# Performance work log

Measured on AMD Instinct MI355X. Metric: run time of the kernel, lower is better.

Reference implementation:

```python
import jax, jax.numpy as jnp
import numpy as np

DECAY_INIT = 0.9
SPECTRAL_RADIUS = 0.5
EPS = 1e-8


def _spectral_normed(W, u, radius):
    # 3 power iterations (no-grad in torch); u, v treated as constants.
    for _ in range(3):
        v = W.T @ u
        v = v / (jnp.linalg.norm(v) + EPS)
        u = W @ v
        u = u / (jnp.linalg.norm(u) + EPS)
    u = jax.lax.stop_gradient(u)
    v = jax.lax.stop_gradient(v)
    sigma = jnp.abs(u @ W @ v)
    return W * (radius / (sigma + EPS))


def setup_inputs() -> dict:
    key = jax.random.key(0)
    ks = jax.random.split(key, 6)
    T, B, D, n = 2048, 8, 1024, 64
    xavier = float(np.sqrt(2.0 / (D + n)))
    x = jax.random.normal(ks[0], (T, B, D), dtype=jnp.float32)
    S0 = jnp.zeros((B, n, n), dtype=jnp.float32)
    W_k = jax.random.normal(ks[1], (n, D), dtype=jnp.float32) * xavier
    W_v = jax.random.normal(ks[2], (n, D), dtype=jnp.float32) * xavier
    W_q = jax.random.normal(ks[3], (n, D), dtype=jnp.float32) * xavier
    u_k = jax.random.normal(ks[4], (n,), dtype=jnp.float32)
    u_k = u_k / (jnp.linalg.norm(u_k) + EPS)
    u_v = jax.random.normal(ks[5], (n,), dtype=jnp.float32)
    u_v = u_v / (jnp.linalg.norm(u_v) + EPS)
    return {"x": x, "S0": S0, "W_k": W_k, "W_v": W_v, "W_q": W_q,
            "u_k": u_k, "u_v": u_v}


def reference(x, S0, W_k, W_v, W_q, u_k, u_v):
    # decay = clamp(0.9, 0, 0.999).item() -> detached constant
    decay = jnp.clip(jnp.float32(DECAY_INIT), 0.0, 0.999)
    Wk = _spectral_normed(W_k, u_k, SPECTRAL_RADIUS)
    Wv = _spectral_normed(W_v, u_v, SPECTRAL_RADIUS)

    # projections: [T, B, n]
    k_all = jnp.einsum('tbd,nd->tbn', x, Wk)
    v_all = jnp.einsum('tbd,nd->tbn', x, Wv)
    q_all = jnp.einsum('tbd,nd->tbn', x, W_q)

    def step(S, kvq):
        k, v, q = kvq  # each [B, n]
        S = decay * S + v[:, :, None] * k[:, None, :]  # [B, n, n]
        sq = jnp.einsum('bij,bj->bi', S, q)
        out = sq * jax.nn.silu(sq)
        return S, (S, out)

    _, (S_seq, output) = jax.lax.scan(step, S0, (k_all, v_all, q_all))
    S_all = jnp.concatenate([S0[None], S_seq], axis=0)  # [T+1, B, n, n]
    return output, S_all
```

## Files before the change

kernel.cpp:

```cpp
#include <hip/hip_runtime.h>
#include <math.h>

#define T_DIM 2048
#define B_DIM 8
#define D_DIM 1024
#define N_DIM 64
#define NCHUNK 16
#define CHUNK_LEN 128
#define DECAY 0.9f
#define EPS 1e-8f
#define RADIUS 0.5f

typedef __attribute__((ext_vector_type(8))) short short8;
typedef __attribute__((ext_vector_type(4))) float f32x4;

static __device__ __forceinline__ unsigned short f2bf(float f) {
    unsigned u = __float_as_uint(f);
    u += 0x7FFFu + ((u >> 16) & 1u);
    return (unsigned short)(u >> 16);
}
static __device__ __forceinline__ float bf2f(unsigned short h) {
    return __uint_as_float(((unsigned)h) << 16);
}

static __device__ __forceinline__ void bar_lgkm() {
    asm volatile("s_waitcnt lgkmcnt(0)" ::: "memory");
    __builtin_amdgcn_s_barrier();
    asm volatile("" ::: "memory");
}

__global__ __launch_bounds__(256)
void gram_kernel(const float* __restrict__ Wk, const float* __restrict__ Wv,
                 float* __restrict__ G) {
    int mat = blockIdx.x >> 6;
    int i   = blockIdx.x & 63;
    const float* W = mat ? Wv : Wk;
    __shared__ float wsr[D_DIM];
    __shared__ float part[4][64];
    int tid = threadIdx.x;
    *(float4*)&wsr[tid * 4] = *(const float4*)(W + (size_t)i * D_DIM + tid * 4);
    __syncthreads();
    int j = tid & 63, p = tid >> 6;
    const float* wj = W + (size_t)j * D_DIM + p * 256;
    const float* wp = wsr + p * 256;
    float acc = 0.f;
    #pragma unroll 16
    for (int k = 0; k < 256; k += 4) {
        float4 a = *(const float4*)(wj + k);
        float4 b = *(const float4*)(wp + k);
        acc += a.x * b.x + a.y * b.y + a.z * b.z + a.w * b.w;
    }
    part[p][j] = acc;
    __syncthreads();
    if (tid < 64)
        G[((size_t)mat * 64 + i) * 64 + tid] =
            part[0][tid] + part[1][tid] + part[2][tid] + part[3][tid];
}

__global__ __launch_bounds__(64)
void power_kernel(const float* __restrict__ G, const float* __restrict__ uk,
                  const float* __restrict__ uv, float* __restrict__ scale_out) {
    __shared__ float Gs[64][65];
    __shared__ float us[64];
    int mat = blockIdx.x;
    int i = threadIdx.x;
    #pragma unroll 8
    for (int r = 0; r < 64; ++r)
        Gs[r][i] = G[((size_t)mat * 64 + r) * 64 + i];
    us[i] = (mat ? uv : uk)[i];
    __syncthreads();
    float sigma = 0.f;
    for (int it = 0; it < 3; ++it) {
        float t = 0.f;
        #pragma unroll
        for (int jj = 0; jj < 64; ++jj)
            t += Gs[i][jj] * us[jj];
        float nv2 = us[i] * t;
        #pragma unroll
        for (int o = 32; o > 0; o >>= 1) nv2 += __shfl_xor(nv2, o, 64);
        float nv = sqrtf(fmaxf(nv2, 0.f));
        float ur = t / (nv + EPS);
        float nu2 = ur * ur;
        #pragma unroll
        for (int o = 32; o > 0; o >>= 1) nu2 += __shfl_xor(nu2, o, 64);
        float nu = sqrtf(nu2);
        if (it == 2) sigma = nu2 / (nu + EPS);
        __syncthreads();
        us[i] = ur / (nu + EPS);
        __syncthreads();
    }
    if (i == 0) scale_out[mat] = RADIUS / (sigma + EPS);
}

__global__ __launch_bounds__(256)
void build_wt_kernel(const float* __restrict__ Wk, const float* __restrict__ Wv,
                     const float* __restrict__ Wq, const float* __restrict__ scale,
                     unsigned short* __restrict__ BPh, unsigned short* __restrict__ BPl) {
    int bid = blockIdx.x;
    int g   = bid >> 3;
    int sub = bid & 7;
    int m   = sub * 256 + threadIdx.x;
    int gm  = g >> 2;
    const float* W = (gm == 0) ? Wk : (gm == 1) ? Wv : Wq;
    float sc = (gm == 0) ? scale[0] : (gm == 1) ? scale[1] : 1.0f;
    int s   = m >> 7;
    int kk  = (m >> 6) & 1;
    int flh = (m >> 4) & 3;
    int fl  = m & 15;
    int row = (g & 3) * 16 + fl;
    int k0  = s * 64 + kk * 32 + flh * 8;
    const float* src = W + (size_t)row * D_DIM + k0;
    float4 a = *(const float4*)src;
    float4 b = *(const float4*)(src + 4);
    float v[8] = {a.x, a.y, a.z, a.w, b.x, b.y, b.z, b.w};
    short8 hv, lv;
    #pragma unroll
    for (int e = 0; e < 8; ++e) {
        float val = v[e] * sc;
        unsigned short hh = f2bf(val);
        hv[e] = (short)hh;
        lv[e] = (short)f2bf(val - bf2f(hh));
    }
    size_t o = (size_t)g * 16384 + (size_t)m * 8;
    *(short8*)(BPh + o) = hv;
    *(short8*)(BPl + o) = lv;
}

#define PBM 32
#define KSTAGE 128
__global__ __launch_bounds__(256)
void proj_mfma_kernel(const float* __restrict__ x,
                      const unsigned short* __restrict__ BPh,
                      const unsigned short* __restrict__ BPl,
                      float* __restrict__ kvq) {
    __shared__ __align__(16) unsigned short ldsA[2][PBM * KSTAGE];
    int tid = threadIdx.x;
    int lane = tid & 63;
    int wv = tid >> 6;
    int fl15 = lane & 15;
    int flh = lane >> 4;
    int rowBase = blockIdx.x * PBM;

    int r_st = tid >> 3;
    int sub  = tid & 7;
    const float* xrow = x + (size_t)(rowBase + r_st) * D_DIM + sub * 8;
    int wb0 = r_st * 256 + ((sub * 16) ^ ((r_st & 7) << 4));
    int wb1 = wb0 + 128;

    const unsigned short* bbh = BPh + (size_t)(wv * 3) * 16384 + lane * 8;
    const unsigned short* bbl = BPl + (size_t)(wv * 3) * 16384 + lane * 8;

    f32x4 acc[2][3];
    #pragma unroll
    for (int mt = 0; mt < 2; ++mt)
        #pragma unroll
        for (int nt = 0; nt < 3; ++nt) acc[mt][nt] = (f32x4)(0.f);

    {
        float4 c0 = *(const float4*)(xrow);
        float4 c1 = *(const float4*)(xrow + 4);
        float4 c2 = *(const float4*)(xrow + 64);
        float4 c3 = *(const float4*)(xrow + 68);
        float v0[8] = {c0.x, c0.y, c0.z, c0.w, c1.x, c1.y, c1.z, c1.w};
        float v1[8] = {c2.x, c2.y, c2.z, c2.w, c3.x, c3.y, c3.z, c3.w};
        short8 h0, h1;
        #pragma unroll
        for (int e = 0; e < 8; ++e) {
            h0[e] = (short)f2bf(v0[e]);
            h1[e] = (short)f2bf(v1[e]);
        }
        char* pH = (char*)&ldsA[0][0];
        *(short8*)(pH + wb0) = h0;
        *(short8*)(pH + wb1) = h1;
    }
    float4 p0 = *(const float4*)(xrow + KSTAGE);
    float4 p1 = *(const float4*)(xrow + KSTAGE + 4);
    float4 p2 = *(const float4*)(xrow + KSTAGE + 64);
    float4 p3 = *(const float4*)(xrow + KSTAGE + 68);
    bar_lgkm();

    #pragma unroll 1
    for (int qt = 0; qt < 8; ++qt) {
        int buf = qt & 1;
        const char* pH = (const char*)&ldsA[buf][0];
        #pragma unroll
        for (int s = 0; s < 2; ++s) {
            int sg = qt * 2 + s;
            short8 bh[2][3], bl[2][3];
            #pragma unroll
            for (int nt = 0; nt < 3; ++nt)
                #pragma unroll
                for (int kk = 0; kk < 2; ++kk) {
                    size_t off = (size_t)nt * 16384 + sg * 1024 + kk * 512;
                    bh[kk][nt] = *(const short8*)(bbh + off);
                    bl[kk][nt] = *(const short8*)(bbl + off);
                }
            #pragma unroll
            for (int kk = 0; kk < 2; ++kk) {
                short8 ah[2];
                #pragma unroll
                for (int mt = 0; mt < 2; ++mt) {
                    int row = mt * 16 + fl15;
                    int off = row * 256 + s * 128 +
                              ((kk * 64 + flh * 16) ^ ((row & 7) << 4));
                    ah[mt] = *(const short8*)(pH + off);
                }
                #pragma unroll
                for (int mt = 0; mt < 2; ++mt)
                    #pragma unroll
                    for (int nt = 0; nt < 3; ++nt) {
                        acc[mt][nt] = __builtin_amdgcn_mfma_f32_16x16x32_bf16(
                            ah[mt], bh[kk][nt], acc[mt][nt], 0, 0, 0);
                        acc[mt][nt] = __builtin_amdgcn_mfma_f32_16x16x32_bf16(
                            ah[mt], bl[kk][nt], acc[mt][nt], 0, 0, 0);
                    }
            }
        }
        float4 q0, q1, q2, q3;
        if (qt < 6) {
            const float* nx = xrow + (qt + 2) * KSTAGE;
            q0 = *(const float4*)(nx);
            q1 = *(const float4*)(nx + 4);
            q2 = *(const float4*)(nx + 64);
            q3 = *(const float4*)(nx + 68);
        }
        if (qt < 7) {
            float v0[8] = {p0.x, p0.y, p0.z, p0.w, p1.x, p1.y, p1.z, p1.w};
            float v1[8] = {p2.x, p2.y, p2.z, p2.w, p3.x, p3.y, p3.z, p3.w};
            short8 h0, h1;
            #pragma unroll
            for (int e = 0; e < 8; ++e) {
                h0[e] = (short)f2bf(v0[e]);
                h1[e] = (short)f2bf(v1[e]);
            }
            char* qH = (char*)&ldsA[buf ^ 1][0];
            *(short8*)(qH + wb0) = h0;
            *(short8*)(qH + wb1) = h1;
        }
        bar_lgkm();
        p0 = q0; p1 = q1; p2 = q2; p3 = q3;
    }

    #pragma unroll
    for (int mt = 0; mt < 2; ++mt)
        #pragma unroll
        for (int nt = 0; nt < 3; ++nt) {
            int col = wv * 48 + nt * 16 + fl15;
            #pragma unroll
            for (int r = 0; r < 4; ++r) {
                int row = rowBase + mt * 16 + flh * 4 + r;
                kvq[(size_t)row * 192 + col] = acc[mt][nt][r];
            }
        }
}

__global__ __launch_bounds__(256)
void carry_init_kernel(const float* __restrict__ kvq,
                       float* __restrict__ S_init) {
    int blk = blockIdx.x;
    int c   = (blk >> 5) + 1;
    int rem = blk & 31;
    int b   = rem >> 2;
    int iq  = rem & 3;
    int i   = iq * 16 + (threadIdx.x >> 4);
    int j4  = (threadIdx.x & 15) * 4;
    int tp  = (c - 1) * CHUNK_LEN;
    float4 s4 = {0.f, 0.f, 0.f, 0.f};
    #pragma unroll 4
    for (int u = 0; u < CHUNK_LEN; ++u) {
        const float* base = kvq + (size_t)((tp + u) * B_DIM + b) * 192;
        float v = base[64 + i];
        float4 k4 = *(const float4*)(base + j4);
        s4.x = __builtin_fmaf(DECAY, s4.x, v * k4.x);
        s4.y = __builtin_fmaf(DECAY, s4.y, v * k4.y);
        s4.z = __builtin_fmaf(DECAY, s4.z, v * k4.z);
        s4.w = __builtin_fmaf(DECAY, s4.w, v * k4.w);
    }
    *(float4*)&S_init[(((size_t)c * B_DIM + b) * 64 + i) * 64 + j4] = s4;
}

#define SC_TILE 8
__global__ __launch_bounds__(256)
void scan_kernel(const float* __restrict__ kvq,
                 const float* __restrict__ S_init,
                 const float* __restrict__ S0,
                 float* __restrict__ out,
                 float* __restrict__ S_all) {
    __shared__ __align__(16) float P[4][SC_TILE][4][20];
    int widL = threadIdx.x >> 6;
    int lane = threadIdx.x & 63;
    int r  = lane >> 4;
    int jq = lane & 15;
    int blk = blockIdx.x;
    int c  = blk >> 5;
    int b  = (blk >> 2) & 7;
    int ig = blk & 3;
    int i0 = ig * 16 + widL * 4;
    int i  = i0 + r;

    int pp   = lane >> 1;
    int ur   = pp >> 2;
    int rr   = pp & 3;
    int half = lane & 1;

    if (c == 0) {
        f32x4 s0v = *(const f32x4*)&S0[((size_t)b * 64 + i) * 64 + jq * 4];
        *(f32x4*)&S_all[(size_t)b * 4096 + (size_t)i * 64 + jq * 4] = s0v;
    }

    f32x4 s = (f32x4)(0.f);
    if (c > 0)
        s = *(const f32x4*)&S_init[(((size_t)c * B_DIM + b) * 64 + i) * 64 + jq * 4];

    int t0 = c * CHUNK_LEN;
    for (int tb = 0; tb < CHUNK_LEN; tb += SC_TILE) {
        #pragma unroll
        for (int u = 0; u < SC_TILE; ++u) {
            int t = t0 + tb + u;
            const float* base = kvq + (size_t)(t * B_DIM + b) * 192;
            f32x4 k4 = *(const f32x4*)(base + jq * 4);
            f32x4 q4 = *(const f32x4*)(base + 128 + jq * 4);
            float v  = base[64 + i];
            s.x = __builtin_fmaf(DECAY, s.x, v * k4.x);
            s.y = __builtin_fmaf(DECAY, s.y, v * k4.y);
            s.z = __builtin_fmaf(DECAY, s.z, v * k4.z);
            s.w = __builtin_fmaf(DECAY, s.w, v * k4.w);
            __builtin_nontemporal_store(
                s, (f32x4*)&S_all[((size_t)(t + 1) * B_DIM + b) * 4096 +
                                  (size_t)i * 64 + jq * 4]);
            P[widL][u][r][jq] = s.x * q4.x + s.y * q4.y + s.z * q4.z + s.w * q4.w;
        }
        const float* pr = &P[widL][ur][rr][half * 8];
        f32x4 a0 = *(const f32x4*)pr;
        f32x4 a1 = *(const f32x4*)(pr + 4);
        float acc = (a0.x + a0.y) + (a0.z + a0.w) + (a1.x + a1.y) + (a1.z + a1.w);
        acc += __shfl_xor(acc, 1, 64);
        if (half == 0) {
            int t = t0 + tb + ur;
            float sg = 1.0f / (1.0f + __expf(-acc));
            out[((size_t)t * B_DIM + b) * 64 + i0 + rr] = acc * acc * sg;
        }
    }
}

extern "C" void kernel_launch(void* const* d_in, const int* in_sizes, int n_in,
                              void* d_out, int out_size, void* d_ws, size_t ws_size,
                              hipStream_t stream) {
    const float* x  = (const float*)d_in[0];
    const float* S0 = (const float*)d_in[1];
    const float* Wk = (const float*)d_in[2];
    const float* Wv = (const float*)d_in[3];
    const float* Wq = (const float*)d_in[4];
    const float* uk = (const float*)d_in[5];
    const float* uv = (const float*)d_in[6];

    float* out   = (float*)d_out;
    float* S_all = out + (size_t)T_DIM * B_DIM * N_DIM;

    float* ws    = (float*)d_ws;
    float* scale = ws;
    float* kvq   = ws + 64;
    unsigned short* BPh = (unsigned short*)(kvq + (size_t)16384 * 192);
    unsigned short* BPl = BPh + (size_t)192 * D_DIM;
    float* S_init = (float*)(BPl + (size_t)192 * D_DIM);
    float* G      = S_init + (size_t)NCHUNK * 32768;

    gram_kernel<<<128, 256, 0, stream>>>(Wk, Wv, G);
    power_kernel<<<2, 64, 0, stream>>>(G, uk, uv, scale);
    build_wt_kernel<<<96, 256, 0, stream>>>(Wk, Wv, Wq, scale, BPh, BPl);
    proj_mfma_kernel<<<T_DIM * B_DIM / PBM, 256, 0, stream>>>(x, BPh, BPl, kvq);
    carry_init_kernel<<<(NCHUNK - 1) * 32, 256, 0, stream>>>(kvq, S_init);
    scan_kernel<<<NCHUNK * B_DIM * 4, 256, 0, stream>>>(kvq, S_init, S0, out, S_all);
}
```

Measured before the change: 118.5 us.

## Split projection K dimension across two blocks and fuse power iteration into weight build

The power-iteration kernel is folded into build_wt_kernel: every Wk/Wv block recomputes the 64x64 power iteration from the Gram matrix, so one launch goes away. The projection kernel now splits the 1024-long reduction into two halves handled by separate blocks, doubling the grid to improve occupancy. The partial sums are combined with float atomics into a kvq buffer that is zeroed by a memset first. The cost is redundant power-iteration work, an extra memset, and atomic write traffic; float atomics also make the summation order nondeterministic.

Result: slower. 131.0 us (+10.6%).

```diff
diff --git a/kernel.cpp b/kernel.cpp
--- a/kernel.cpp
+++ b/kernel.cpp
@@ -57,58 +57,65 @@
             part[0][tid] + part[1][tid] + part[2][tid] + part[3][tid];
 }
 
-__global__ __launch_bounds__(64)
-void power_kernel(const float* __restrict__ G, const float* __restrict__ uk,
-                  const float* __restrict__ uv, float* __restrict__ scale_out) {
+__global__ __launch_bounds__(256)
+void build_wt_kernel(const float* __restrict__ Wk, const float* __restrict__ Wv,
+                     const float* __restrict__ Wq, const float* __restrict__ G,
+                     const float* __restrict__ uk, const float* __restrict__ uv,
+                     unsigned short* __restrict__ BPh, unsigned short* __restrict__ BPl) {
     __shared__ float Gs[64][65];
-    __shared__ float us[64];
-    int mat = blockIdx.x;
-    int i = threadIdx.x;
-    #pragma unroll 8
-    for (int r = 0; r < 64; ++r)
-        Gs[r][i] = G[((size_t)mat * 64 + r) * 64 + i];
-    us[i] = (mat ? uv : uk)[i];
-    __syncthreads();
-    float sigma = 0.f;
-    for (int it = 0; it < 3; ++it) {
-        float t = 0.f;
-        #pragma unroll
-        for (int jj = 0; jj < 64; ++jj)
-            t += Gs[i][jj] * us[jj];
-        float nv2 = us[i] * t;
-        #pragma unroll
-        for (int o = 32; o > 0; o >>= 1) nv2 += __shfl_xor(nv2, o, 64);
-        float nv = sqrtf(fmaxf(nv2, 0.f));
-        float ur = t / (nv + EPS);
-        float nu2 = ur * ur;
-        #pragma unroll
-        for (int o = 32; o > 0; o >>= 1) nu2 += __shfl_xor(nu2, o, 64);
-        float nu = sqrtf(nu2);
-        if (it == 2) sigma = nu2 / (nu + EPS);
-        __syncthreads();
-        us[i] = ur / (nu + EPS);
-        __syncthreads();
-    }
-    if (i == 0) scale_out[mat] = RADIUS / (sigma + EPS);
-}
-
-__global__ __launch_bounds__(256)
-void build_wt_kernel(const float* __restrict__ Wk, const float* __restrict__ Wv,
-                     const float* __restrict__ Wq, const float* __restrict__ scale,
-                     unsigned short* __restrict__ BPh, unsigned short* __restrict__ BPl) {
+    __shared__ float us_s[64];
+    __shared__ float sc_s;
     int bid = blockIdx.x;
     int g   = bid >> 3;
-    int sub = bid & 7;
-    int m   = sub * 256 + threadIdx.x;
     int gm  = g >> 2;
+    int tid = threadIdx.x;
+
+    if (gm < 2) {
+        #pragma unroll
+        for (int e = 0; e < 16; ++e) {
+            int idx = e * 256 + tid;
+            Gs[idx >> 6][idx & 63] = G[(size_t)gm * 4096 + idx];
+        }
+        if (tid < 64) us_s[tid] = (gm ? uv : uk)[tid];
+        __syncthreads();
+        if (tid < 64) {
+            int i = tid;
+            float sigma = 0.f;
+            for (int it = 0; it < 3; ++it) {
+                float t = 0.f;
+                #pragma unroll
+                for (int jj = 0; jj < 64; ++jj)
+                    t += Gs[i][jj] * us_s[jj];
+                float nv2 = us_s[i] * t;
+                #pragma unroll
+                for (int o = 32; o > 0; o >>= 1) nv2 += __shfl_xor(nv2, o, 64);
+                float nv = sqrtf(fmaxf(nv2, 0.f));
+                float ur = t / (nv + EPS);
+                float nu2 = ur * ur;
+                #pragma unroll
+                for (int o = 32; o > 0; o >>= 1) nu2 += __shfl_xor(nu2, o, 64);
+                float nu = sqrtf(nu2);
+                if (it == 2) sigma = nu2 / (nu + EPS);
+                us_s[i] = ur / (nu + EPS);
+            }
+            if (tid == 0) sc_s = RADIUS / (sigma + EPS);
+        }
+    } else {
+        if (tid == 0) sc_s = 1.0f;
+    }
+    __syncthreads();
+    float sc = sc_s;
+
     const float* W = (gm == 0) ? Wk : (gm == 1) ? Wv : Wq;
-    float sc = (gm == 0) ? scale[0] : (gm == 1) ? scale[1] : 1.0f;
-    int s   = m >> 7;
-    int kk  = (m >> 6) & 1;
-    int flh = (m >> 4) & 3;
-    int fl  = m & 15;
-    int row = (g & 3) * 16 + fl;
-    int k0  = s * 64 + kk * 32 + flh * 8;
+    for (int sub8 = 0; sub8 < 1; ++sub8) { }
+    int subb = bid & 7;
+    int m    = subb * 256 + tid;
+    int s    = m >> 7;
+    int kk   = (m >> 6) & 1;
+    int flh  = (m >> 4) & 3;
+    int fl   = m & 15;
+    int row  = (g & 3) * 16 + fl;
+    int k0   = s * 64 + kk * 32 + flh * 8;
     const float* src = W + (size_t)row * D_DIM + k0;
     float4 a = *(const float4*)src;
     float4 b = *(const float4*)(src + 4);
@@ -139,16 +146,18 @@
     int wv = tid >> 6;
     int fl15 = lane & 15;
     int flh = lane >> 4;
-    int rowBase = blockIdx.x * PBM;
+    int mb   = blockIdx.x >> 1;
+    int half = blockIdx.x & 1;
+    int rowBase = mb * PBM;
 
     int r_st = tid >> 3;
     int sub  = tid & 7;
-    const float* xrow = x + (size_t)(rowBase + r_st) * D_DIM + sub * 8;
+    const float* xrow = x + (size_t)(rowBase + r_st) * D_DIM + half * 512 + sub * 8;
     int wb0 = r_st * 256 + ((sub * 16) ^ ((r_st & 7) << 4));
     int wb1 = wb0 + 128;
 
-    const unsigned short* bbh = BPh + (size_t)(wv * 3) * 16384 + lane * 8;
-    const unsigned short* bbl = BPl + (size_t)(wv * 3) * 16384 + lane * 8;
+    const unsigned short* bbh = BPh + (size_t)(wv * 3) * 16384 + half * 8192 + lane * 8;
+    const unsigned short* bbl = BPl + (size_t)(wv * 3) * 16384 + half * 8192 + lane * 8;
 
     f32x4 acc[2][3];
     #pragma unroll
@@ -180,7 +189,7 @@
     bar_lgkm();
 
     #pragma unroll 1
-    for (int qt = 0; qt < 8; ++qt) {
+    for (int qt = 0; qt < 4; ++qt) {
         int buf = qt & 1;
         const char* pH = (const char*)&ldsA[buf][0];
         #pragma unroll
@@ -217,14 +226,14 @@
             }
         }
         float4 q0, q1, q2, q3;
-        if (qt < 6) {
+        if (qt < 2) {
             const float* nx = xrow + (qt + 2) * KSTAGE;
             q0 = *(const float4*)(nx);
             q1 = *(const float4*)(nx + 4);
             q2 = *(const float4*)(nx + 64);
             q3 = *(const float4*)(nx + 68);
         }
-        if (qt < 7) {
+        if (qt < 3) {
             float v0[8] = {p0.x, p0.y, p0.z, p0.w, p1.x, p1.y, p1.z, p1.w};
             float v1[8] = {p2.x, p2.y, p2.z, p2.w, p3.x, p3.y, p3.z, p3.w};
             short8 h0, h1;
@@ -249,7 +258,7 @@
             #pragma unroll
             for (int r = 0; r < 4; ++r) {
                 int row = rowBase + mt * 16 + flh * 4 + r;
-                kvq[(size_t)row * 192 + col] = acc[mt][nt][r];
+                unsafeAtomicAdd(&kvq[(size_t)row * 192 + col], acc[mt][nt][r]);
             }
         }
 }
@@ -358,17 +367,16 @@
     float* S_all = out + (size_t)T_DIM * B_DIM * N_DIM;
 
     float* ws    = (float*)d_ws;
-    float* scale = ws;
-    float* kvq   = ws + 64;
+    float* kvq   = ws;
     unsigned short* BPh = (unsigned short*)(kvq + (size_t)16384 * 192);
     unsigned short* BPl = BPh + (size_t)192 * D_DIM;
     float* S_init = (float*)(BPl + (size_t)192 * D_DIM);
     float* G      = S_init + (size_t)NCHUNK * 32768;
 
+    hipMemsetAsync(kvq, 0, (size_t)16384 * 192 * sizeof(float), stream);
     gram_kernel<<<128, 256, 0, stream>>>(Wk, Wv, G);
-    power_kernel<<<2, 64, 0, stream>>>(G, uk, uv, scale);
-    build_wt_kernel<<<96, 256, 0, stream>>>(Wk, Wv, Wq, scale, BPh, BPl);
-    proj_mfma_kernel<<<T_DIM * B_DIM / PBM, 256, 0, stream>>>(x, BPh, BPl, kvq);
+    build_wt_kernel<<<96, 256, 0, stream>>>(Wk, Wv, Wq, G, uk, uv, BPh, BPl);
+    proj_mfma_kernel<<<T_DIM * B_DIM / PBM * 2, 256, 0, stream>>>(x, BPh, BPl, kvq);
     carry_init_kernel<<<(NCHUNK - 1) * 32, 256, 0, stream>>>(kvq, S_init);
     scan_kernel<<<NCHUNK * B_DIM * 4, 256, 0, stream>>>(kvq, S_init, S0, out, S_all);
 }
```
